# Performance work log

Hardware: AMD Instinct MI355X
Metric: run time of the kernel (lower is better)

Reference implementation:

```python
import jax, jax.numpy as jnp
import numpy as np

N_NODES = 100000
N_EDGES = 1600000
D_IN = 64
D_OUT = 64
K_ORDERS = 4  # K+1 Chebyshev orders (K=3)


def setup_inputs() -> dict:
    key = jax.random.key(0)
    k1, k2, k3, k4, k5 = jax.random.split(key, 5)
    x = jax.random.normal(k1, (N_NODES, D_IN), dtype=jnp.float32)
    edge_index = jax.random.randint(k2, (2, N_EDGES), 0, N_NODES, dtype=jnp.int64)
    edge_attr = jax.random.uniform(k3, (N_EDGES,), dtype=jnp.float32)
    weight = jax.random.normal(k4, (K_ORDERS, D_IN, D_OUT), dtype=jnp.float32) * 0.05
    bias = jax.random.normal(k5, (D_OUT,), dtype=jnp.float32) * 0.05
    return {"x": x, "edge_index": edge_index, "edge_attr": edge_attr,
            "weight": weight, "bias": bias}


def reference(x, edge_index, edge_attr, weight, bias):
    n = x.shape[0]
    row, col = edge_index[0], edge_index[1]
    # degree = number of edges per destination node (row)
    deg = jax.ops.segment_sum(jnp.ones_like(edge_attr), row, num_segments=n)
    dinv = jnp.where(deg > 0, deg ** -0.5, 0.0)
    # negative normalized adjacency acting as rescaled Laplacian
    lap = -dinv[row] * edge_attr * dinv[col]  # [E]

    def spmm(h):  # out[row] += lap * h[col]
        return jax.ops.segment_sum(lap[:, None] * h[col], row, num_segments=n)

    k_orders = weight.shape[0]
    tx0 = x
    out = tx0 @ weight[0]
    tx1 = spmm(tx0)
    out = out + tx1 @ weight[1]
    for k in range(2, k_orders):  # small fixed K, fine to unroll
        tx2 = 2.0 * spmm(tx1) - tx0
        out = out + tx2 @ weight[k]
        tx0, tx1 = tx1, tx2
    return out + bias
```

## Files before the change

### kernel.cpp

```cpp
#include <hip/hip_runtime.h>

#define D 64
#define BLK 256

#define NBSHIFT 9
#define NODES_PER_BKT 512
#define TA 4096
#define CVT_BLOCKS 512

typedef unsigned int uint32;
typedef __attribute__((ext_vector_type(8))) short bf16x8;
typedef __attribute__((ext_vector_type(4))) float f32x4;

__device__ inline uint32 f2bf_u(float f) {
    uint32 u = __float_as_uint(f);
    u += 0x7FFFu + ((u >> 16) & 1u);
    return u >> 16;
}

__global__ void pre_kernel(const float* __restrict__ x, uint2* __restrict__ xb, int n4,
                           const float* __restrict__ W, uint4* __restrict__ Wf,
                           const int* __restrict__ row, uint32* __restrict__ bcount, int E) {
    int bid = blockIdx.x;
    if (bid < CVT_BLOCKS) {
        int stride = CVT_BLOCKS * BLK;
        for (int i = bid * BLK + threadIdx.x; i < n4; i += stride) {
            float4 v = ((const float4*)x)[i];
            uint2 pack;
            pack.x = f2bf_u(v.x) | (f2bf_u(v.y) << 16);
            pack.y = f2bf_u(v.z) | (f2bf_u(v.w) << 16);
            xb[i] = pack;
        }
        return;
    }
    if (bid < CVT_BLOCKS + 8) {
        int tid = (bid - CVT_BLOCKS) * 256 + threadIdx.x;
        int l = tid & 63;
        int g = tid >> 6;
        int kh = g & 1;
        int t = (g >> 1) & 3;
        int w = g >> 3;
        int n = t * 16 + (l & 15);
        int kbase = kh * 32 + (l >> 4) * 8;
        uint32 pk[4];
        #pragma unroll
        for (int i = 0; i < 4; ++i) {
            uint32 b0 = f2bf_u(W[(size_t)w * 4096 + (size_t)(kbase + 2 * i) * 64 + n]);
            uint32 b1 = f2bf_u(W[(size_t)w * 4096 + (size_t)(kbase + 2 * i + 1) * 64 + n]);
            pk[i] = b0 | (b1 << 16);
        }
        Wf[tid] = make_uint4(pk[0], pk[1], pk[2], pk[3]);
        return;
    }
    __shared__ uint32 h[256];
    int tid = threadIdx.x;
    h[tid] = 0;
    __syncthreads();
    int base = (bid - CVT_BLOCKS - 8) * TA;
    int end = min(base + TA, E);
    for (int e = base + tid; e < end; e += 256)
        atomicAdd(&h[(uint32)row[e] >> NBSHIFT], 1u);
    __syncthreads();
    if (h[tid]) atomicAdd(&bcount[tid], h[tid]);
}

__global__ void binA_kernel(const int* __restrict__ row, const int* __restrict__ col,
                            const float* __restrict__ attr, const uint32* __restrict__ bcount,
                            uint32* __restrict__ gcursor, int2* __restrict__ binned, int E) {
    __shared__ uint32 hist[256], baseg[256], lstart[256], lcur[256];
    __shared__ int2 stage[TA];
    __shared__ unsigned char sbkt[TA];
    int tid = threadIdx.x;
    int tile = blockIdx.x * TA;
    hist[tid] = 0;
    __syncthreads();

    uint32 px[16], py[16], bk[16];
    #pragma unroll
    for (int k = 0; k < 16; ++k) {
        int e = tile + k * 256 + tid;
        bk[k] = 0xFFFFFFFFu;
        if (e < E) {
            int r = row[e], c = col[e];
            uint32 b = (uint32)r >> NBSHIFT;
            bk[k] = b;
            px[k] = ((uint32)(r & (NODES_PER_BKT - 1)) << 17) | (uint32)c;
            py[k] = __float_as_uint(attr[e]);
            atomicAdd(&hist[b], 1u);
        }
    }
    __syncthreads();
    uint32 bc = bcount[tid];
    lcur[tid] = bc;
    __syncthreads();
    for (int off = 1; off < 256; off <<= 1) {
        uint32 t = (tid >= off) ? lcur[tid - off] : 0u;
        __syncthreads();
        lcur[tid] += t;
        __syncthreads();
    }
    uint32 gexcl = lcur[tid] - bc;
    if (hist[tid] > 0) baseg[tid] = gexcl + atomicAdd(&gcursor[tid], hist[tid]);
    __syncthreads();
    lcur[tid] = hist[tid];
    __syncthreads();
    for (int off = 1; off < 256; off <<= 1) {
        uint32 t = (tid >= off) ? lcur[tid - off] : 0u;
        __syncthreads();
        lcur[tid] += t;
        __syncthreads();
    }
    lstart[tid] = lcur[tid] - hist[tid];
    lcur[tid] = lstart[tid];
    __syncthreads();
    #pragma unroll
    for (int k = 0; k < 16; ++k) {
        if (bk[k] != 0xFFFFFFFFu) {
            uint32 pos = atomicAdd(&lcur[bk[k]], 1u);
            stage[pos] = make_int2((int)px[k], (int)py[k]);
            sbkt[pos] = (unsigned char)bk[k];
        }
    }
    __syncthreads();
    int cnt = min(TA, E - tile);
    for (int i = tid; i < cnt; i += 256) {
        uint32 b = sbkt[i];
        uint32 dst = baseg[b] + (uint32)i - lstart[b];
        binned[dst] = stage[i];
    }
}

__global__ void binBdeg_kernel(const int2* __restrict__ binned, const uint32* __restrict__ bcount,
                               uint32* __restrict__ rowptr, float* __restrict__ dinv,
                               int N, int E) {
    __shared__ uint32 cnt[NODES_PER_BKT];
    __shared__ uint32 ps[256];
    int b = blockIdx.x;
    int tid = threadIdx.x;
    cnt[tid] = 0;
    cnt[tid + 256] = 0;
    uint32 bc = bcount[tid];
    ps[tid] = bc;
    __syncthreads();
    for (int off = 1; off < 256; off <<= 1) {
        uint32 t = (tid >= off) ? ps[tid - off] : 0u;
        __syncthreads();
        ps[tid] += t;
        __syncthreads();
    }
    uint32 incl_b = ps[b];
    uint32 bc_b = bcount[b];
    uint32 start = incl_b - bc_b, end = incl_b;
    __syncthreads();
    for (uint32 i = start + tid; i < end; i += 256)
        atomicAdd(&cnt[(uint32)binned[i].x >> 17], 1u);
    __syncthreads();
    uint32 c0 = cnt[2 * tid], c1 = cnt[2 * tid + 1];
    ps[tid] = c0 + c1;
    __syncthreads();
    for (int off = 1; off < 256; off <<= 1) {
        uint32 t = (tid >= off) ? ps[tid - off] : 0u;
        __syncthreads();
        ps[tid] += t;
        __syncthreads();
    }
    uint32 pexcl = ps[tid] - (c0 + c1);
    int base = b << NBSHIFT;
    int n0 = base + 2 * tid, n1 = n0 + 1;
    if (n0 < N) {
        rowptr[n0] = start + pexcl;
        dinv[n0] = c0 ? rsqrtf((float)c0) : 0.0f;
    }
    if (n1 < N) {
        rowptr[n1] = start + pexcl + c0;
        dinv[n1] = c1 ? rsqrtf((float)c1) : 0.0f;
    }
    if (b == (int)gridDim.x - 1 && tid == 0) rowptr[N] = (uint32)E;
}

__global__ void binBsort_kernel(const int2* __restrict__ binned, const uint32* __restrict__ bcount,
                                const uint32* __restrict__ rowptr, const float* __restrict__ dinv,
                                int2* __restrict__ pairs, int N) {
    __shared__ uint32 lcur[NODES_PER_BKT];
    __shared__ float ldin[NODES_PER_BKT];
    __shared__ uint32 ps[256];
    int b = blockIdx.x;
    int tid = threadIdx.x;
    int base = b << NBSHIFT;
    uint32 bc = bcount[tid];
    ps[tid] = bc;
    __syncthreads();
    for (int off = 1; off < 256; off <<= 1) {
        uint32 t = (tid >= off) ? ps[tid - off] : 0u;
        __syncthreads();
        ps[tid] += t;
        __syncthreads();
    }
    uint32 incl_b = ps[b];
    uint32 start = incl_b - bcount[b], end = incl_b;
    for (int t = tid; t < NODES_PER_BKT; t += 256) {
        int node = base + t;
        lcur[t] = (node < N) ? (rowptr[node] - start) : 0u;
        ldin[t] = (node < N) ? dinv[node] : 0.0f;
    }
    __syncthreads();
    for (uint32 i = start + tid; i < end; i += 256) {
        int2 rec = binned[i];
        uint32 x = (uint32)rec.x;
        uint32 rl = x >> 17;
        uint32 c = x & 0x1FFFFu;
        float lap = -ldin[rl] * __int_as_float(rec.y) * dinv[c];
        uint32 pos = atomicAdd(&lcur[rl], 1u);
        pairs[start + pos] = make_int2((int)(c << 7), __float_as_int(lap));
    }
}

#define LOAD16(J, END, ESAFE, M0, M1, H0, H1)                          \
    {                                                                  \
        uint32 i0_ = (J) + q, i1_ = (J) + 8 + q;                       \
        uint32 c0_ = (i0_ < (END)) ? i0_ : (ESAFE);                    \
        uint32 c1_ = (i1_ < (END)) ? i1_ : (ESAFE);                    \
        M0 = pairs[c0_];                                               \
        M1 = pairs[c1_];                                               \
        H0 = *(const uint4*)(hb + (uint32)M0.x + off);                 \
        H1 = *(const uint4*)(hb + (uint32)M1.x + off);                 \
    }

#define FMA16(J, END, M0, M1, H0, H1, A)                               \
    {                                                                  \
        uint32 i0_ = (J) + q, i1_ = (J) + 8 + q;                       \
        float l0_ = (i0_ < (END)) ? __int_as_float(M0.y) : 0.0f;       \
        float l1_ = (i1_ < (END)) ? __int_as_float(M1.y) : 0.0f;       \
        A[0] += l0_ * __uint_as_float(H0.x << 16);                     \
        A[1] += l0_ * __uint_as_float(H0.x & 0xFFFF0000u);             \
        A[2] += l0_ * __uint_as_float(H0.y << 16);                     \
        A[3] += l0_ * __uint_as_float(H0.y & 0xFFFF0000u);             \
        A[4] += l0_ * __uint_as_float(H0.z << 16);                     \
        A[5] += l0_ * __uint_as_float(H0.z & 0xFFFF0000u);             \
        A[6] += l0_ * __uint_as_float(H0.w << 16);                     \
        A[7] += l0_ * __uint_as_float(H0.w & 0xFFFF0000u);             \
        A[0] += l1_ * __uint_as_float(H1.x << 16);                     \
        A[1] += l1_ * __uint_as_float(H1.x & 0xFFFF0000u);             \
        A[2] += l1_ * __uint_as_float(H1.y << 16);                     \
        A[3] += l1_ * __uint_as_float(H1.y & 0xFFFF0000u);             \
        A[4] += l1_ * __uint_as_float(H1.z << 16);                     \
        A[5] += l1_ * __uint_as_float(H1.z & 0xFFFF0000u);             \
        A[6] += l1_ * __uint_as_float(H1.w << 16);                     \
        A[7] += l1_ * __uint_as_float(H1.w & 0xFFFF0000u);             \
    }

__global__ void spmm2r_kernel(const uint32* __restrict__ rowptr, const int2* __restrict__ pairs,
                              const char* __restrict__ hb, const uint4* __restrict__ prev,
                              uint4* __restrict__ out, float scale, int N) {
    int wid = blockIdx.x * 4 + (threadIdx.x >> 6);
    int nA = wid * 2;
    if (nA >= N) return;
    int lane = threadIdx.x & 63;
    int q = lane >> 3;
    int sub = lane & 7;
    int off = sub * 16;
    bool hasB = (nA + 1 < N);

    uint2 rpA = *(const uint2*)(rowptr + nA);
    uint32 eBr = hasB ? rowptr[nA + 2] : rpA.y;
    uint32 jA   = __builtin_amdgcn_readfirstlane(rpA.x);
    uint32 endA = __builtin_amdgcn_readfirstlane(rpA.y);
    uint32 jB   = endA;
    uint32 endB = __builtin_amdgcn_readfirstlane(eBr);
    uint32 esA = (endA > jA) ? endA - 1 : 0u;
    uint32 esB = (endB > jB) ? endB - 1 : 0u;

    int nq = nA + (q & 1);
    uint4 pv = make_uint4(0u, 0u, 0u, 0u);
    if (prev && q < 2 && nq < N) pv = prev[(size_t)nq * 8 + sub];

    float aA[8], aB[8];
    #pragma unroll
    for (int i = 0; i < 8; ++i) { aA[i] = 0.0f; aB[i] = 0.0f; }

    int2 mA0, mA1, mA2, mA3, mB0, mB1, mB2, mB3;
    uint4 hA0, hA1, hA2, hA3, hB0, hB1, hB2, hB3;

    bool dA = (jA + 16 < endA);
    bool dB = (jB + 16 < endB);

    LOAD16(jA, endA, esA, mA0, mA1, hA0, hA1);
    LOAD16(jB, endB, esB, mB0, mB1, hB0, hB1);
    if (dA) LOAD16(jA + 16, endA, esA, mA2, mA3, hA2, hA3);
    if (dB) LOAD16(jB + 16, endB, esB, mB2, mB3, hB2, hB3);
    FMA16(jA, endA, mA0, mA1, hA0, hA1, aA);
    FMA16(jB, endB, mB0, mB1, hB0, hB1, aB);
    if (dA) FMA16(jA + 16, endA, mA2, mA3, hA2, hA3, aA);
    if (dB) FMA16(jB + 16, endB, mB2, mB3, hB2, hB3, aB);
    jA += 32;
    jB += 32;

    while (jA < endA) {
        LOAD16(jA, endA, esA, mA0, mA1, hA0, hA1);
        FMA16(jA, endA, mA0, mA1, hA0, hA1, aA);
        if (jA + 16 < endA) {
            LOAD16(jA + 16, endA, esA, mA2, mA3, hA2, hA3);
            FMA16(jA + 16, endA, mA2, mA3, hA2, hA3, aA);
        }
        jA += 32;
    }
    while (jB < endB) {
        LOAD16(jB, endB, esB, mB0, mB1, hB0, hB1);
        FMA16(jB, endB, mB0, mB1, hB0, hB1, aB);
        if (jB + 16 < endB) {
            LOAD16(jB + 16, endB, esB, mB2, mB3, hB2, hB3);
            FMA16(jB + 16, endB, mB2, mB3, hB2, hB3, aB);
        }
        jB += 32;
    }

    #pragma unroll
    for (int i = 0; i < 8; ++i) {
        aA[i] += __shfl_xor(aA[i], 8);
        aA[i] += __shfl_xor(aA[i], 16);
        aA[i] += __shfl_xor(aA[i], 32);
        aB[i] += __shfl_xor(aB[i], 8);
        aB[i] += __shfl_xor(aB[i], 16);
        aB[i] += __shfl_xor(aB[i], 32);
    }

    if (q < 2 && nq < N) {
        bool isB = (q == 1);
        float r[8];
        #pragma unroll
        for (int i = 0; i < 8; ++i) r[i] = scale * (isB ? aB[i] : aA[i]);
        if (prev) {
            r[0] -= __uint_as_float(pv.x << 16);
            r[1] -= __uint_as_float(pv.x & 0xFFFF0000u);
            r[2] -= __uint_as_float(pv.y << 16);
            r[3] -= __uint_as_float(pv.y & 0xFFFF0000u);
            r[4] -= __uint_as_float(pv.z << 16);
            r[5] -= __uint_as_float(pv.z & 0xFFFF0000u);
            r[6] -= __uint_as_float(pv.w << 16);
            r[7] -= __uint_as_float(pv.w & 0xFFFF0000u);
        }
        uint4 pack;
        pack.x = f2bf_u(r[0]) | (f2bf_u(r[1]) << 16);
        pack.y = f2bf_u(r[2]) | (f2bf_u(r[3]) << 16);
        pack.z = f2bf_u(r[4]) | (f2bf_u(r[5]) << 16);
        pack.w = f2bf_u(r[6]) | (f2bf_u(r[7]) << 16);
        out[(size_t)nq * 8 + sub] = pack;
    }
}

__global__ void gemm_mfma(const uint4* __restrict__ h0, const uint4* __restrict__ h1,
                          const uint4* __restrict__ h2, const uint4* __restrict__ h3,
                          const uint4* __restrict__ Wf, const float* __restrict__ bias,
                          float* __restrict__ out, int N) {
    int tid = threadIdx.x;
    int wave = tid >> 6;
    int lane = tid & 63;
    int quad = lane >> 4;
    int lo = lane & 15;
    int m0 = blockIdx.x * 64 + wave * 16;
    int mrow = m0 + lo;
    int mclamp = min(mrow, N - 1);

    f32x4 acc[4] = {{0.f,0.f,0.f,0.f},{0.f,0.f,0.f,0.f},{0.f,0.f,0.f,0.f},{0.f,0.f,0.f,0.f}};
    const uint4* hs[4] = { h0, h1, h2, h3 };
    #pragma unroll
    for (int w = 0; w < 4; ++w) {
        union { uint4 u; bf16x8 v; } a0, a1;
        a0.u = hs[w][(size_t)mclamp * 8 + quad];
        a1.u = hs[w][(size_t)mclamp * 8 + 4 + quad];
        #pragma unroll
        for (int t = 0; t < 4; ++t) {
            union { uint4 u; bf16x8 v; } b0, b1;
            b0.u = Wf[(w * 8 + t * 2 + 0) * 64 + lane];
            b1.u = Wf[(w * 8 + t * 2 + 1) * 64 + lane];
            acc[t] = __builtin_amdgcn_mfma_f32_16x16x32_bf16(a0.v, b0.v, acc[t], 0, 0, 0);
            acc[t] = __builtin_amdgcn_mfma_f32_16x16x32_bf16(a1.v, b1.v, acc[t], 0, 0, 0);
        }
    }
    #pragma unroll
    for (int t = 0; t < 4; ++t) {
        int col = t * 16 + lo;
        float bv = bias[col];
        #pragma unroll
        for (int r = 0; r < 4; ++r) {
            int rowi = m0 + quad * 4 + r;
            if (rowi < N) out[(size_t)rowi * 64 + col] = acc[t][r] + bv;
        }
    }
}

extern "C" void kernel_launch(void* const* d_in, const int* in_sizes, int n_in,
                              void* d_out, int out_size, void* d_ws, size_t ws_size,
                              hipStream_t stream) {
    const float* x    = (const float*)d_in[0];
    const int*   ei   = (const int*)d_in[1];
    const float* attr = (const float*)d_in[2];
    const float* W    = (const float*)d_in[3];
    const float* bias = (const float*)d_in[4];
    float* out = (float*)d_out;

    const int N = in_sizes[0] / D;
    const int E = in_sizes[1] / 2;
    const int* row = ei;
    const int* col = ei + E;
    const int NB = (N + NODES_PER_BKT - 1) >> NBSHIFT;

    char* p = (char*)d_ws;
    int2*     pairs   = (int2*)p;                p += (size_t)E * 8;
    uint2*    xb      = (uint2*)p;               p += (size_t)N * D * 2;
    uint2*    T1      = (uint2*)p;               p += (size_t)N * D * 2;
    uint2*    T2      = (uint2*)p;               p += (size_t)N * D * 2;
    uint2*    T3      = (uint2*)p;               p += (size_t)N * D * 2;
    uint4*    Wf      = (uint4*)p;               p += 2048 * 16;
    uint32*   rowptr  = (uint32*)p;              p += (size_t)(N + 1) * 4;
    uint32*   bcount  = (uint32*)p;              p += 256 * 4;
    uint32*   gcursor = (uint32*)p;              p += 256 * 4;
    float*    dinv    = (float*)p;
    int2*     binned  = (int2*)T3;

    const int gSp = (N + 7) / 8;
    const int gGm = (N + 63) / 64;
    const int gTile = (E + TA - 1) / TA;

    hipMemsetAsync(bcount, 0, 512 * 4, stream);
    pre_kernel<<<CVT_BLOCKS + 8 + gTile, BLK, 0, stream>>>(x, xb, N * D / 4, W, Wf,
                                                           row, bcount, E);
    binA_kernel<<<gTile, 256, 0, stream>>>(row, col, attr, bcount, gcursor, binned, E);
    binBdeg_kernel<<<NB, 256, 0, stream>>>(binned, bcount, rowptr, dinv, N, E);
    binBsort_kernel<<<NB, 256, 0, stream>>>(binned, bcount, rowptr, dinv, pairs, N);

    spmm2r_kernel<<<gSp, BLK, 0, stream>>>(rowptr, pairs, (const char*)xb, nullptr, (uint4*)T1, 1.0f, N);
    spmm2r_kernel<<<gSp, BLK, 0, stream>>>(rowptr, pairs, (const char*)T1, (const uint4*)xb, (uint4*)T2, 2.0f, N);
    spmm2r_kernel<<<gSp, BLK, 0, stream>>>(rowptr, pairs, (const char*)T2, (const uint4*)T1, (uint4*)T3, 2.0f, N);
    gemm_mfma<<<gGm, BLK, 0, stream>>>((const uint4*)xb, (const uint4*)T1, (const uint4*)T2,
                                       (const uint4*)T3, Wf, bias, out, N);
}
```

Measured before the change: 284.8 us.

## Fuse final SpMM order into MFMA GEMM kernel via LDS staging

Merges the third Chebyshev SpMM with the final GEMM. Each wave computes T3 for its 16 rows in a serial loop of node pairs, stages the bf16 results in shared memory, and feeds them straight into the MFMA accumulation. This removes one kernel launch and the global write and re-read of T3. In exchange, each wave processes 8 node pairs sequentially, so the grid has 8x fewer waves for that SpMM. That cuts the parallelism available to hide gather latency.

```diff
diff --git a/kernel.cpp b/kernel.cpp
--- a/kernel.cpp
+++ b/kernel.cpp
@@ -249,6 +249,60 @@
         A[7] += l1_ * __uint_as_float(H1.w & 0xFFFF0000u);             \
     }
 
+#define SPMM_BURST(NA, AA, AB)                                                        \
+    {                                                                                 \
+        bool hasB_ = ((NA) + 1 < N);                                                  \
+        uint2 rpA_ = *(const uint2*)(rowptr + (NA));                                  \
+        uint32 eBr_ = hasB_ ? rowptr[(NA) + 2] : rpA_.y;                              \
+        uint32 jA = __builtin_amdgcn_readfirstlane(rpA_.x);                           \
+        uint32 endA = __builtin_amdgcn_readfirstlane(rpA_.y);                         \
+        uint32 jB = endA;                                                             \
+        uint32 endB = __builtin_amdgcn_readfirstlane(eBr_);                           \
+        uint32 esA = (endA > jA) ? endA - 1 : 0u;                                     \
+        uint32 esB = (endB > jB) ? endB - 1 : 0u;                                     \
+        int2 mA0, mA1, mA2, mA3, mB0, mB1, mB2, mB3;                                  \
+        uint4 hA0, hA1, hA2, hA3, hB0, hB1, hB2, hB3;                                 \
+        bool dA = (jA + 16 < endA);                                                   \
+        bool dB = (jB + 16 < endB);                                                   \
+        LOAD16(jA, endA, esA, mA0, mA1, hA0, hA1);                                    \
+        LOAD16(jB, endB, esB, mB0, mB1, hB0, hB1);                                    \
+        if (dA) LOAD16(jA + 16, endA, esA, mA2, mA3, hA2, hA3);                       \
+        if (dB) LOAD16(jB + 16, endB, esB, mB2, mB3, hB2, hB3);                       \
+        FMA16(jA, endA, mA0, mA1, hA0, hA1, AA);                                      \
+        FMA16(jB, endB, mB0, mB1, hB0, hB1, AB);                                      \
+        if (dA) FMA16(jA + 16, endA, mA2, mA3, hA2, hA3, AA);                         \
+        if (dB) FMA16(jB + 16, endB, mB2, mB3, hB2, hB3, AB);                         \
+        jA += 32;                                                                     \
+        jB += 32;                                                                     \
+        while (jA < endA) {                                                           \
+            LOAD16(jA, endA, esA, mA0, mA1, hA0, hA1);                                \
+            FMA16(jA, endA, mA0, mA1, hA0, hA1, AA);                                  \
+            if (jA + 16 < endA) {                                                     \
+                LOAD16(jA + 16, endA, esA, mA2, mA3, hA2, hA3);                       \
+                FMA16(jA + 16, endA, mA2, mA3, hA2, hA3, AA);                         \
+            }                                                                         \
+            jA += 32;                                                                 \
+        }                                                                             \
+        while (jB < endB) {                                                           \
+            LOAD16(jB, endB, esB, mB0, mB1, hB0, hB1);                                \
+            FMA16(jB, endB, mB0, mB1, hB0, hB1, AB);                                  \
+            if (jB + 16 < endB) {                                                     \
+                LOAD16(jB + 16, endB, esB, mB2, mB3, hB2, hB3);                       \
+                FMA16(jB + 16, endB, mB2, mB3, hB2, hB3, AB);                         \
+            }                                                                         \
+            jB += 32;                                                                 \
+        }                                                                             \
+        _Pragma("unroll")                                                             \
+        for (int i_ = 0; i_ < 8; ++i_) {                                              \
+            AA[i_] += __shfl_xor(AA[i_], 8);                                          \
+            AA[i_] += __shfl_xor(AA[i_], 16);                                         \
+            AA[i_] += __shfl_xor(AA[i_], 32);                                         \
+            AB[i_] += __shfl_xor(AB[i_], 8);                                          \
+            AB[i_] += __shfl_xor(AB[i_], 16);                                         \
+            AB[i_] += __shfl_xor(AB[i_], 32);                                         \
+        }                                                                             \
+    }
+
 __global__ void spmm2r_kernel(const uint32* __restrict__ rowptr, const int2* __restrict__ pairs,
                               const char* __restrict__ hb, const uint4* __restrict__ prev,
                               uint4* __restrict__ out, float scale, int N) {
@@ -259,16 +313,6 @@
     int q = lane >> 3;
     int sub = lane & 7;
     int off = sub * 16;
-    bool hasB = (nA + 1 < N);
-
-    uint2 rpA = *(const uint2*)(rowptr + nA);
-    uint32 eBr = hasB ? rowptr[nA + 2] : rpA.y;
-    uint32 jA   = __builtin_amdgcn_readfirstlane(rpA.x);
-    uint32 endA = __builtin_amdgcn_readfirstlane(rpA.y);
-    uint32 jB   = endA;
-    uint32 endB = __builtin_amdgcn_readfirstlane(eBr);
-    uint32 esA = (endA > jA) ? endA - 1 : 0u;
-    uint32 esB = (endB > jB) ? endB - 1 : 0u;
 
     int nq = nA + (q & 1);
     uint4 pv = make_uint4(0u, 0u, 0u, 0u);
@@ -278,51 +322,7 @@
     #pragma unroll
     for (int i = 0; i < 8; ++i) { aA[i] = 0.0f; aB[i] = 0.0f; }
 
-    int2 mA0, mA1, mA2, mA3, mB0, mB1, mB2, mB3;
-    uint4 hA0, hA1, hA2, hA3, hB0, hB1, hB2, hB3;
-
-    bool dA = (jA + 16 < endA);
-    bool dB = (jB + 16 < endB);
-
-    LOAD16(jA, endA, esA, mA0, mA1, hA0, hA1);
-    LOAD16(jB, endB, esB, mB0, mB1, hB0, hB1);
-    if (dA) LOAD16(jA + 16, endA, esA, mA2, mA3, hA2, hA3);
-    if (dB) LOAD16(jB + 16, endB, esB, mB2, mB3, hB2, hB3);
-    FMA16(jA, endA, mA0, mA1, hA0, hA1, aA);
-    FMA16(jB, endB, mB0, mB1, hB0, hB1, aB);
-    if (dA) FMA16(jA + 16, endA, mA2, mA3, hA2, hA3, aA);
-    if (dB) FMA16(jB + 16, endB, mB2, mB3, hB2, hB3, aB);
-    jA += 32;
-    jB += 32;
-
-    while (jA < endA) {
-        LOAD16(jA, endA, esA, mA0, mA1, hA0, hA1);
-        FMA16(jA, endA, mA0, mA1, hA0, hA1, aA);
-        if (jA + 16 < endA) {
-            LOAD16(jA + 16, endA, esA, mA2, mA3, hA2, hA3);
-            FMA16(jA + 16, endA, mA2, mA3, hA2, hA3, aA);
-        }
-        jA += 32;
-    }
-    while (jB < endB) {
-        LOAD16(jB, endB, esB, mB0, mB1, hB0, hB1);
-        FMA16(jB, endB, mB0, mB1, hB0, hB1, aB);
-        if (jB + 16 < endB) {
-            LOAD16(jB + 16, endB, esB, mB2, mB3, hB2, hB3);
-            FMA16(jB + 16, endB, mB2, mB3, hB2, hB3, aB);
-        }
-        jB += 32;
-    }
-
-    #pragma unroll
-    for (int i = 0; i < 8; ++i) {
-        aA[i] += __shfl_xor(aA[i], 8);
-        aA[i] += __shfl_xor(aA[i], 16);
-        aA[i] += __shfl_xor(aA[i], 32);
-        aB[i] += __shfl_xor(aB[i], 8);
-        aB[i] += __shfl_xor(aB[i], 16);
-        aB[i] += __shfl_xor(aB[i], 32);
-    }
+    SPMM_BURST(nA, aA, aB);
 
     if (q < 2 && nq < N) {
         bool isB = (q == 1);
@@ -348,23 +348,72 @@
     }
 }
 
-__global__ void gemm_mfma(const uint4* __restrict__ h0, const uint4* __restrict__ h1,
-                          const uint4* __restrict__ h2, const uint4* __restrict__ h3,
-                          const uint4* __restrict__ Wf, const float* __restrict__ bias,
-                          float* __restrict__ out, int N) {
+__global__ void spmm_gemm_kernel(const uint32* __restrict__ rowptr, const int2* __restrict__ pairs,
+                                 const char* __restrict__ hb , const uint4* __restrict__ prev ,
+                                 const uint4* __restrict__ h0, const uint4* __restrict__ h1,
+                                 const uint4* __restrict__ h2,
+                                 const uint4* __restrict__ Wf, const float* __restrict__ bias,
+                                 float* __restrict__ out, int N) {
+    __shared__ uint4 lds3[64][8];
     int tid = threadIdx.x;
     int wave = tid >> 6;
     int lane = tid & 63;
+    int q = lane >> 3;
+    int sub = lane & 7;
+    int off = sub * 16;
+    int wrow = blockIdx.x * 64 + wave * 16;
+
+    #pragma unroll 1
+    for (int t = 0; t < 8; ++t) {
+        int nA = wrow + 2 * t;
+        int ls = wave * 16 + 2 * t;
+        int nq = nA + (q & 1);
+        if (nA >= N) {
+            if (q < 2) lds3[ls + (q & 1)][sub] = make_uint4(0u, 0u, 0u, 0u);
+            continue;
+        }
+        uint4 pv = make_uint4(0u, 0u, 0u, 0u);
+        if (q < 2 && nq < N) pv = prev[(size_t)nq * 8 + sub];
+
+        float aA[8], aB[8];
+        #pragma unroll
+        for (int i = 0; i < 8; ++i) { aA[i] = 0.0f; aB[i] = 0.0f; }
+
+        SPMM_BURST(nA, aA, aB);
+
+        if (q < 2) {
+            uint4 pack = make_uint4(0u, 0u, 0u, 0u);
+            if (nq < N) {
+                bool isB = (q == 1);
+                float r[8];
+                #pragma unroll
+                for (int i = 0; i < 8; ++i) r[i] = 2.0f * (isB ? aB[i] : aA[i]);
+                r[0] -= __uint_as_float(pv.x << 16);
+                r[1] -= __uint_as_float(pv.x & 0xFFFF0000u);
+                r[2] -= __uint_as_float(pv.y << 16);
+                r[3] -= __uint_as_float(pv.y & 0xFFFF0000u);
+                r[4] -= __uint_as_float(pv.z << 16);
+                r[5] -= __uint_as_float(pv.z & 0xFFFF0000u);
+                r[6] -= __uint_as_float(pv.w << 16);
+                r[7] -= __uint_as_float(pv.w & 0xFFFF0000u);
+                pack.x = f2bf_u(r[0]) | (f2bf_u(r[1]) << 16);
+                pack.y = f2bf_u(r[2]) | (f2bf_u(r[3]) << 16);
+                pack.z = f2bf_u(r[4]) | (f2bf_u(r[5]) << 16);
+                pack.w = f2bf_u(r[6]) | (f2bf_u(r[7]) << 16);
+            }
+            lds3[ls + (q & 1)][sub] = pack;
+        }
+    }
+
     int quad = lane >> 4;
     int lo = lane & 15;
-    int m0 = blockIdx.x * 64 + wave * 16;
-    int mrow = m0 + lo;
+    int mrow = wrow + lo;
     int mclamp = min(mrow, N - 1);
 
     f32x4 acc[4] = {{0.f,0.f,0.f,0.f},{0.f,0.f,0.f,0.f},{0.f,0.f,0.f,0.f},{0.f,0.f,0.f,0.f}};
-    const uint4* hs[4] = { h0, h1, h2, h3 };
+    const uint4* hs[3] = { h0, h1, h2 };
     #pragma unroll
-    for (int w = 0; w < 4; ++w) {
+    for (int w = 0; w < 3; ++w) {
         union { uint4 u; bf16x8 v; } a0, a1;
         a0.u = hs[w][(size_t)mclamp * 8 + quad];
         a1.u = hs[w][(size_t)mclamp * 8 + 4 + quad];
@@ -377,13 +426,26 @@
             acc[t] = __builtin_amdgcn_mfma_f32_16x16x32_bf16(a1.v, b1.v, acc[t], 0, 0, 0);
         }
     }
+    {
+        union { uint4 u; bf16x8 v; } a0, a1;
+        a0.u = lds3[wave * 16 + lo][quad];
+        a1.u = lds3[wave * 16 + lo][4 + quad];
+        #pragma unroll
+        for (int t = 0; t < 4; ++t) {
+            union { uint4 u; bf16x8 v; } b0, b1;
+            b0.u = Wf[(3 * 8 + t * 2 + 0) * 64 + lane];
+            b1.u = Wf[(3 * 8 + t * 2 + 1) * 64 + lane];
+            acc[t] = __builtin_amdgcn_mfma_f32_16x16x32_bf16(a0.v, b0.v, acc[t], 0, 0, 0);
+            acc[t] = __builtin_amdgcn_mfma_f32_16x16x32_bf16(a1.v, b1.v, acc[t], 0, 0, 0);
+        }
+    }
     #pragma unroll
     for (int t = 0; t < 4; ++t) {
         int col = t * 16 + lo;
         float bv = bias[col];
         #pragma unroll
         for (int r = 0; r < 4; ++r) {
-            int rowi = m0 + quad * 4 + r;
+            int rowi = wrow + quad * 4 + r;
             if (rowi < N) out[(size_t)rowi * 64 + col] = acc[t][r] + bv;
         }
     }
@@ -410,16 +472,15 @@
     uint2*    xb      = (uint2*)p;               p += (size_t)N * D * 2;
     uint2*    T1      = (uint2*)p;               p += (size_t)N * D * 2;
     uint2*    T2      = (uint2*)p;               p += (size_t)N * D * 2;
-    uint2*    T3      = (uint2*)p;               p += (size_t)N * D * 2;
+    int2*     binned  = (int2*)p;                p += (size_t)N * D * 2;
     uint4*    Wf      = (uint4*)p;               p += 2048 * 16;
     uint32*   rowptr  = (uint32*)p;              p += (size_t)(N + 1) * 4;
     uint32*   bcount  = (uint32*)p;              p += 256 * 4;
     uint32*   gcursor = (uint32*)p;              p += 256 * 4;
     float*    dinv    = (float*)p;
-    int2*     binned  = (int2*)T3;
 
     const int gSp = (N + 7) / 8;
-    const int gGm = (N + 63) / 64;
+    const int gFg = (N + 63) / 64;
     const int gTile = (E + TA - 1) / TA;
 
     hipMemsetAsync(bcount, 0, 512 * 4, stream);
@@ -431,7 +492,7 @@
 
     spmm2r_kernel<<<gSp, BLK, 0, stream>>>(rowptr, pairs, (const char*)xb, nullptr, (uint4*)T1, 1.0f, N);
     spmm2r_kernel<<<gSp, BLK, 0, stream>>>(rowptr, pairs, (const char*)T1, (const uint4*)xb, (uint4*)T2, 2.0f, N);
-    spmm2r_kernel<<<gSp, BLK, 0, stream>>>(rowptr, pairs, (const char*)T2, (const uint4*)T1, (uint4*)T3, 2.0f, N);
-    gemm_mfma<<<gGm, BLK, 0, stream>>>((const uint4*)xb, (const uint4*)T1, (const uint4*)T2,
-                                       (const uint4*)T3, Wf, bias, out, N);
-}
+    spmm_gemm_kernel<<<gFg, BLK, 0, stream>>>(rowptr, pairs, (const char*)T2, (const uint4*)T1,
+                                              (const uint4*)xb, (const uint4*)T1, (const uint4*)T2,
+                                              Wf, bias, out, N);
+}
```

Result: slower. 294.7 us (+3.5%).
